# Performance work log

Hardware: AMD Instinct MI355X
Metric: run time of the kernel (lower is better)

Reference implementation:

```python
import jax, jax.numpy as jnp
import numpy as np

N_CHUNKS = 2


def _sig_kernel(X, Y):
    """Signature kernel PDE solution K[:, -1, -1].
    X: (A, M, D), Y: (A, N, D). Effective grid is (M, N) (the original CUDA
    kernel's last row/col read OOB and are trimmed away).
    Recurrence: K[i,j] = K[i-1,j] + K[i,j-1] + K[i-1,j-1]*(inc[i-1,j-1]-1),
    K[0,:] = K[:,0] = 1.  For a fixed row i this is a cumulative sum:
    K[i,j] = 1 + cumsum_j( K[i-1,j] + K[i-1,j-1]*(inc-1) ).
    """
    dX = X[:, 1:] - X[:, :-1]                      # (A, M-1, D)
    dY = Y[:, 1:] - Y[:, :-1]                      # (A, N-1, D)
    inc = jnp.einsum('amd,and->amn', dX, dY)       # (A, M-1, N-1)
    n = inc.shape[2]
    dtype = inc.dtype

    def solve(inc_b):                              # inc_b: (M-1, N-1)
        row0 = jnp.ones(n + 1, dtype)

        def step(prev_row, inc_row):
            # c[j] = K[i-1,j+1] + K[i-1,j]*(inc[j]-1),  j = 0..n-1
            c = prev_row[1:] + prev_row[:-1] * (inc_row - 1.0)
            new_row = jnp.concatenate(
                [jnp.ones((1,), dtype), 1.0 + jnp.cumsum(c)])
            return new_row, None

        last_row, _ = jax.lax.scan(step, row0, inc_b)
        return last_row[-1]

    return jax.vmap(solve)(inc)                    # (A,)


def _sig_distance(x, y):
    return jnp.mean(_sig_kernel(x, x) + _sig_kernel(y, y)
                    - 2.0 * _sig_kernel(x, y))


def _sig_loss(X, Y, n_chunks=N_CHUNKS):
    if n_chunks == 1:
        return _sig_distance(X, Y)
    dist = jnp.zeros((), X.dtype)
    for k in range(2, n_chunks + 1):
        Xc = jnp.array_split(X, k, axis=1)
        Yc = jnp.array_split(Y, k, axis=1)
        for x1, x2, y1, y2 in zip(Xc[:-1], Xc[1:], Yc[:-1], Yc[1:]):
            dist = dist + _sig_distance(jnp.concatenate([x1, x2], axis=1),
                                        jnp.concatenate([y1, y2], axis=1))
    return dist


def setup_inputs() -> dict:
    key = jax.random.key(0)
    kx, ky = jax.random.split(key)
    A, L, D = 256, 256, 32
    SCALE = 0.02  # keep exp growth of the PDE solution in fp32 range
    X = SCALE * jax.random.normal(kx, (A, L, D), dtype=jnp.float32)
    Y = SCALE * jax.random.normal(ky, (A, L, D), dtype=jnp.float32)
    return {"X": X, "Y": Y}


def reference(X, Y):
    return _sig_loss(X, Y, n_chunks=N_CHUNKS)
```

## Files before the change

### kernel.cpp

```cpp
#include <hip/hip_runtime.h>


typedef _Float16 half8 __attribute__((ext_vector_type(8)));
typedef float f32x4_t __attribute__((ext_vector_type(4)));

#define DPP_ADD(v, ctrl, rmask)                                               \
    ((v) + __int_as_float(__builtin_amdgcn_update_dpp(                        \
               0, __float_as_int(v), (ctrl), (rmask), 0xF, true)))

#define INV2048 4.8828125e-4f

__global__ __launch_bounds__(64)
__attribute__((amdgpu_waves_per_eu(1, 1)))
void sig_pde(const float* __restrict__ X,
             const float* __restrict__ Y,
             float* __restrict__ partial) {
    const int bid = blockIdx.x;
    const int p = bid >> 8;
    const int a = bid & 255;
    const float* __restrict__ U = (p == 1) ? Y : X;
    const float* __restrict__ V = (p == 0) ? X : Y;
    U += (size_t)a * 256 * 32;
    V += (size_t)a * 256 * 32;
    const int lane = threadIdx.x;
    const int m16 = lane & 15;
    const int g2 = (lane >> 4) * 2;

    __shared__ __attribute__((aligned(16))) float incD[2][16 * 260];

    const float4* U4 = (const float4*)U;
    const float4* V4 = (const float4*)V;

    half8 bh[16], bl[16];
#pragma unroll
    for (int t = 0; t < 16; ++t) {
        int col = t * 16 + m16;
        int cp = (col + 1 < 256) ? col + 1 : 255;
        float4 lo0 = V4[col * 8 + g2], lo1 = V4[col * 8 + g2 + 1];
        float4 hi0 = V4[cp * 8 + g2],  hi1 = V4[cp * 8 + g2 + 1];
        float d[8] = {hi0.x - lo0.x, hi0.y - lo0.y, hi0.z - lo0.z, hi0.w - lo0.w,
                      hi1.x - lo1.x, hi1.y - lo1.y, hi1.z - lo1.z, hi1.w - lo1.w};
#pragma unroll
        for (int i = 0; i < 8; ++i) {
            _Float16 h = (_Float16)d[i];
            bh[t][i] = h;
            bl[t][i] = (_Float16)((d[i] - (float)h) * 2048.0f);
        }
    }

    float kp0 = 1.0f, kp1 = 1.0f, kp2 = 1.0f, kp3 = 1.0f;

    auto loadA = [&](int blk, float4 (&dst)[4]) {
        int r0 = blk * 16 + m16;
        int r1 = (r0 + 1 < 256) ? r0 + 1 : 255;
        dst[0] = U4[r0 * 8 + g2];
        dst[1] = U4[r0 * 8 + g2 + 1];
        dst[2] = U4[r1 * 8 + g2];
        dst[3] = U4[r1 * 8 + g2 + 1];
    };
    auto makeAhAl = [&](const float4 (&src)[4], half8& ah, half8& al) {
        float d[8] = {src[2].x - src[0].x, src[2].y - src[0].y,
                      src[2].z - src[0].z, src[2].w - src[0].w,
                      src[3].x - src[1].x, src[3].y - src[1].y,
                      src[3].z - src[1].z, src[3].w - src[1].w};
#pragma unroll
        for (int i = 0; i < 8; ++i) {
            _Float16 h = (_Float16)d[i];
            ah[i] = h;
            al[i] = (_Float16)((d[i] - (float)h) * 2048.0f);
        }
    };

    auto scan_row = [&](float4 mv) {
        float kn = __int_as_float(__builtin_amdgcn_update_dpp(
            0, __float_as_int(kp0), 0x130 , 0xF, 0xF, true));
        float c0 = fmaf(kp0, mv.x, kp1);
        float c1 = fmaf(kp1, mv.y, kp2);
        float c2 = fmaf(kp2, mv.z, kp3);
        float c3 = (lane == 63) ? 0.0f : fmaf(kp3, mv.w, kn);
        float L0 = c0, L1 = L0 + c1, L2 = L1 + c2;
        float T = L2 + c3;
        float S = T;
        S = DPP_ADD(S, 0x111, 0xF);
        S = DPP_ADD(S, 0x112, 0xF);
        S = DPP_ADD(S, 0x114, 0xF);
        S = DPP_ADD(S, 0x118, 0xF);
        S = DPP_ADD(S, 0x142, 0xA);
        S = DPP_ADD(S, 0x143, 0xC);
        float E = S - T;
        kp0 = 1.0f + E;
        kp1 = 1.0f + E + L0;
        kp2 = 1.0f + E + L1;
        kp3 = 1.0f + E + L2;
    };

    const f32x4_t zero4 = {0.0f, 0.0f, 0.0f, 0.0f};
    const f32x4_t mone4 = {-1.0f, -1.0f, -1.0f, -1.0f};
    const int rb = (lane >> 4) << 2;

    float4 A[4];
    loadA(0, A);
    half8 ah, al;
    makeAhAl(A, ah, al);
    {
        float* __restrict__ wb = incD[0];
#pragma unroll
        for (int t = 0; t < 16; ++t) {
            f32x4_t a2a = __builtin_amdgcn_mfma_f32_16x16x32_f16(
                ah, bl[t], zero4, 0, 0, 0);
            f32x4_t a2b = __builtin_amdgcn_mfma_f32_16x16x32_f16(
                al, bh[t], zero4, 0, 0, 0);
            f32x4_t a1 = __builtin_amdgcn_mfma_f32_16x16x32_f16(
                ah, bh[t], mone4, 0, 0, 0);
            f32x4_t s = a2a + a2b;
            int cc = t * 16 + m16;
            wb[(rb + 0) * 260 + cc] = fmaf(s[0], INV2048, a1[0]);
            wb[(rb + 1) * 260 + cc] = fmaf(s[1], INV2048, a1[1]);
            wb[(rb + 2) * 260 + cc] = fmaf(s[2], INV2048, a1[2]);
            wb[(rb + 3) * 260 + cc] = fmaf(s[3], INV2048, a1[3]);
        }
    }

#pragma clang loop unroll(disable)
    for (int b = 1; b < 16; ++b) {
        loadA(b, A);
        const float4* rp = (const float4*)incD[(b - 1) & 1];
        float* __restrict__ wb = incD[b & 1];
        makeAhAl(A, ah, al);
        float4 w[4];
        w[0] = rp[0 * 65 + lane]; w[1] = rp[1 * 65 + lane];
        w[2] = rp[2 * 65 + lane]; w[3] = rp[3 * 65 + lane];
#pragma unroll
        for (int k = 0; k < 16; ++k) {
            f32x4_t a2a = __builtin_amdgcn_mfma_f32_16x16x32_f16(
                ah, bl[k], zero4, 0, 0, 0);
            f32x4_t a2b = __builtin_amdgcn_mfma_f32_16x16x32_f16(
                al, bh[k], zero4, 0, 0, 0);
            f32x4_t a1 = __builtin_amdgcn_mfma_f32_16x16x32_f16(
                ah, bh[k], mone4, 0, 0, 0);
            scan_row(w[k & 3]);
            if (k + 4 < 16) w[k & 3] = rp[(k + 4) * 65 + lane];
            f32x4_t s = a2a + a2b;
            int cc = k * 16 + m16;
            wb[(rb + 0) * 260 + cc] = fmaf(s[0], INV2048, a1[0]);
            wb[(rb + 1) * 260 + cc] = fmaf(s[1], INV2048, a1[1]);
            wb[(rb + 2) * 260 + cc] = fmaf(s[2], INV2048, a1[2]);
            wb[(rb + 3) * 260 + cc] = fmaf(s[3], INV2048, a1[3]);
        }
    }

    {
        const float4* rp = (const float4*)incD[1];
        float4 w[4];
        w[0] = rp[0 * 65 + lane]; w[1] = rp[1 * 65 + lane];
        w[2] = rp[2 * 65 + lane]; w[3] = rp[3 * 65 + lane];
#pragma unroll
        for (int k = 0; k < 15; ++k) {
            scan_row(w[k & 3]);
            if (k + 4 < 15) w[k & 3] = rp[(k + 4) * 65 + lane];
        }
    }

    if (lane == 63) {
        partial[bid] = (p == 2 ? -2.0f : 1.0f) * kp3;
    }
}

__global__ __launch_bounds__(256) void sig_reduce(const float* __restrict__ partial,
                                                  float* __restrict__ out) {
    const int t = threadIdx.x;
    float v = partial[t] + partial[t + 256] + partial[t + 512];
#pragma unroll
    for (int ofs = 32; ofs > 0; ofs >>= 1) v += __shfl_down(v, ofs);
    __shared__ float ws[4];
    if ((t & 63) == 0) ws[t >> 6] = v;
    __syncthreads();
    if (t == 0) out[0] = (ws[0] + ws[1] + ws[2] + ws[3]) * (1.0f / 256.0f);
}

extern "C" void kernel_launch(void* const* d_in, const int* in_sizes, int n_in,
                              void* d_out, int out_size, void* d_ws, size_t ws_size,
                              hipStream_t stream) {
    const float* X = (const float*)d_in[0];
    const float* Y = (const float*)d_in[1];
    float* partial = (float*)d_ws;
    sig_pde<<<dim3(768), dim3(64), 0, stream>>>(X, Y, partial);
    sig_reduce<<<dim3(1), dim3(256), 0, stream>>>(partial, (float*)d_out);
}
```

Measured before the change: 47.73 us.

## Unroll ping-pong by two, prefetch next A block, chain MFMA accumulations

Splits the double-buffered LDS array into two separate buffers and unrolls the block loop by two so buffer addresses are compile-time constants. The global load for the next A block is issued one phase ahead, giving it a whole phase to land. The two low-part MFMAs are chained through the accumulator instead of being summed with a vector add. This adds code size and register pressure, and the chained MFMA adds a dependency between the two products.

```diff
diff --git a/kernel.cpp b/kernel.cpp
--- a/kernel.cpp
+++ b/kernel.cpp
@@ -26,7 +26,8 @@
     const int m16 = lane & 15;
     const int g2 = (lane >> 4) * 2;
 
-    __shared__ __attribute__((aligned(16))) float incD[2][16 * 260];
+    __shared__ __attribute__((aligned(16))) float incA[16 * 260];
+    __shared__ __attribute__((aligned(16))) float incB[16 * 260];
 
     const float4* U4 = (const float4*)U;
     const float4* V4 = (const float4*)V;
@@ -99,67 +100,100 @@
     const int rb = (lane >> 4) << 2;
 
     float4 A[4];
-    loadA(0, A);
     half8 ah, al;
-    makeAhAl(A, ah, al);
-    {
-        float* __restrict__ wb = incD[0];
+
+    auto produce_only = [&](float* __restrict__ wb) {
 #pragma unroll
         for (int t = 0; t < 16; ++t) {
-            f32x4_t a2a = __builtin_amdgcn_mfma_f32_16x16x32_f16(
+            f32x4_t a2 = __builtin_amdgcn_mfma_f32_16x16x32_f16(
                 ah, bl[t], zero4, 0, 0, 0);
-            f32x4_t a2b = __builtin_amdgcn_mfma_f32_16x16x32_f16(
-                al, bh[t], zero4, 0, 0, 0);
+            a2 = __builtin_amdgcn_mfma_f32_16x16x32_f16(al, bh[t], a2, 0, 0, 0);
             f32x4_t a1 = __builtin_amdgcn_mfma_f32_16x16x32_f16(
                 ah, bh[t], mone4, 0, 0, 0);
-            f32x4_t s = a2a + a2b;
             int cc = t * 16 + m16;
-            wb[(rb + 0) * 260 + cc] = fmaf(s[0], INV2048, a1[0]);
-            wb[(rb + 1) * 260 + cc] = fmaf(s[1], INV2048, a1[1]);
-            wb[(rb + 2) * 260 + cc] = fmaf(s[2], INV2048, a1[2]);
-            wb[(rb + 3) * 260 + cc] = fmaf(s[3], INV2048, a1[3]);
-        }
-    }
-
-#pragma clang loop unroll(disable)
-    for (int b = 1; b < 16; ++b) {
-        loadA(b, A);
-        const float4* rp = (const float4*)incD[(b - 1) & 1];
-        float* __restrict__ wb = incD[b & 1];
-        makeAhAl(A, ah, al);
-        float4 w[4];
-        w[0] = rp[0 * 65 + lane]; w[1] = rp[1 * 65 + lane];
-        w[2] = rp[2 * 65 + lane]; w[3] = rp[3 * 65 + lane];
+            wb[(rb + 0) * 260 + cc] = fmaf(a2[0], INV2048, a1[0]);
+            wb[(rb + 1) * 260 + cc] = fmaf(a2[1], INV2048, a1[1]);
+            wb[(rb + 2) * 260 + cc] = fmaf(a2[2], INV2048, a1[2]);
+            wb[(rb + 3) * 260 + cc] = fmaf(a2[3], INV2048, a1[3]);
+        }
+    };
+
+    auto phase = [&](const float* __restrict__ rd, float* __restrict__ wb) {
+        const float4* rp = (const float4*)rd;
+        float4 w0 = rp[0 * 65 + lane], w1 = rp[1 * 65 + lane];
+        float4 w2 = rp[2 * 65 + lane], w3 = rp[3 * 65 + lane];
 #pragma unroll
         for (int k = 0; k < 16; ++k) {
-            f32x4_t a2a = __builtin_amdgcn_mfma_f32_16x16x32_f16(
+            f32x4_t a2 = __builtin_amdgcn_mfma_f32_16x16x32_f16(
                 ah, bl[k], zero4, 0, 0, 0);
-            f32x4_t a2b = __builtin_amdgcn_mfma_f32_16x16x32_f16(
-                al, bh[k], zero4, 0, 0, 0);
+            a2 = __builtin_amdgcn_mfma_f32_16x16x32_f16(al, bh[k], a2, 0, 0, 0);
             f32x4_t a1 = __builtin_amdgcn_mfma_f32_16x16x32_f16(
                 ah, bh[k], mone4, 0, 0, 0);
-            scan_row(w[k & 3]);
-            if (k + 4 < 16) w[k & 3] = rp[(k + 4) * 65 + lane];
-            f32x4_t s = a2a + a2b;
+            float4 mv;
+            if ((k & 3) == 0) mv = w0;
+            else if ((k & 3) == 1) mv = w1;
+            else if ((k & 3) == 2) mv = w2;
+            else mv = w3;
+            scan_row(mv);
+            if (k + 4 < 16) {
+                float4 nw = rp[(k + 4) * 65 + lane];
+                if ((k & 3) == 0) w0 = nw;
+                else if ((k & 3) == 1) w1 = nw;
+                else if ((k & 3) == 2) w2 = nw;
+                else w3 = nw;
+            }
+            f32x4_t s;
+            s[0] = fmaf(a2[0], INV2048, a1[0]);
+            s[1] = fmaf(a2[1], INV2048, a1[1]);
+            s[2] = fmaf(a2[2], INV2048, a1[2]);
+            s[3] = fmaf(a2[3], INV2048, a1[3]);
             int cc = k * 16 + m16;
-            wb[(rb + 0) * 260 + cc] = fmaf(s[0], INV2048, a1[0]);
-            wb[(rb + 1) * 260 + cc] = fmaf(s[1], INV2048, a1[1]);
-            wb[(rb + 2) * 260 + cc] = fmaf(s[2], INV2048, a1[2]);
-            wb[(rb + 3) * 260 + cc] = fmaf(s[3], INV2048, a1[3]);
-        }
+            wb[(rb + 0) * 260 + cc] = s[0];
+            wb[(rb + 1) * 260 + cc] = s[1];
+            wb[(rb + 2) * 260 + cc] = s[2];
+            wb[(rb + 3) * 260 + cc] = s[3];
+        }
+    };
+
+    auto scan_tail = [&](const float* __restrict__ rd) {
+        const float4* rp = (const float4*)rd;
+        float4 w0 = rp[0 * 65 + lane], w1 = rp[1 * 65 + lane];
+        float4 w2 = rp[2 * 65 + lane], w3 = rp[3 * 65 + lane];
+#pragma unroll
+        for (int k = 0; k < 15; ++k) {
+            float4 mv;
+            if ((k & 3) == 0) mv = w0;
+            else if ((k & 3) == 1) mv = w1;
+            else if ((k & 3) == 2) mv = w2;
+            else mv = w3;
+            scan_row(mv);
+            if (k + 4 < 15) {
+                float4 nw = rp[(k + 4) * 65 + lane];
+                if ((k & 3) == 0) w0 = nw;
+                else if ((k & 3) == 1) w1 = nw;
+                else if ((k & 3) == 2) w2 = nw;
+                else w3 = nw;
+            }
+        }
+    };
+
+    loadA(0, A);
+    makeAhAl(A, ah, al);
+    loadA(1, A);
+    produce_only(incA);
+
+#pragma clang loop unroll(disable)
+    for (int bb = 0; bb < 7; ++bb) {
+        makeAhAl(A, ah, al);
+        loadA(2 * bb + 2, A);
+        phase(incA, incB);
+        makeAhAl(A, ah, al);
+        loadA(2 * bb + 3, A);
+        phase(incB, incA);
     }
-
-    {
-        const float4* rp = (const float4*)incD[1];
-        float4 w[4];
-        w[0] = rp[0 * 65 + lane]; w[1] = rp[1 * 65 + lane];
-        w[2] = rp[2 * 65 + lane]; w[3] = rp[3 * 65 + lane];
-#pragma unroll
-        for (int k = 0; k < 15; ++k) {
-            scan_row(w[k & 3]);
-            if (k + 4 < 15) w[k & 3] = rp[(k + 4) * 65 + lane];
-        }
-    }
+    makeAhAl(A, ah, al);
+    phase(incA, incB);
+    scan_tail(incB);
 
     if (lane == 63) {
         partial[bid] = (p == 2 ? -2.0f : 1.0f) * kp3;
```

After: 43.12 us. -9.7%, faster.
